# Optimization experiments

Measured on AMD Instinct MI355X. Metric: run time of the kernel, lower is better.

## Reference

```python
import jax, jax.numpy as jnp
import numpy as np
import math

B = 128      # bandwidth
BATCH = 2048 # flat batch (samples x channels)


def _dlt_weights(Bv):
    # Driscoll-Healy quadrature weights, length 2B
    k = np.arange(2 * Bv)
    p = np.arange(Bv)
    C = 2.0 / Bv * np.sin(np.pi * (2 * k + 1) / (4.0 * Bv))
    S = np.sin(np.outer(2 * k + 1, 2 * p + 1) * np.pi / (4.0 * Bv))  # [2B,B]
    return C * (S @ (1.0 / (2 * p + 1)))


def _idct_matrix(N):
    k = np.arange(N)[:, None]
    n = np.arange(N)[None, :]
    DI = np.cos(np.pi * n * (k + 0.5) / N)
    DI[:, 0] *= np.sqrt(1.0 / N)
    DI[:, 1:] *= np.sqrt(2.0 / N)
    return DI


def _idst_matrix(N):
    k = np.arange(N)[:, None]
    n = np.arange(N)[None, :]
    DI = np.sin(np.pi * (n + 1) * (k + 0.5) / N)
    DI[:, N - 1] = (-1.0) ** np.arange(N)
    DI[:, :N - 1] *= np.sqrt(2.0 / N)
    DI[:, N - 1] *= np.sqrt(1.0 / N)
    return DI


def _little_half(Bv):
    # Wigner little-d at beta=pi/2 via 3-term recurrence (vectorized over m,n)
    Bm1 = Bv - 1
    s2 = np.sqrt(2.0)
    d = np.zeros((Bv, 2 * Bv - 1, 2 * Bv - 1))
    d[0, Bm1, Bm1] = 1.0
    d[1, Bm1 - 1, Bm1 - 1] = 0.5
    d[1, Bm1 - 1, Bm1] = 1.0 / s2
    d[1, Bm1 - 1, Bm1 + 1] = 0.5
    d[1, Bm1, Bm1 - 1] = -1.0 / s2
    d[1, Bm1, Bm1 + 1] = 1.0 / s2
    d[1, Bm1 + 1, Bm1 - 1] = 0.5
    d[1, Bm1 + 1, Bm1] = -1.0 / s2
    d[1, Bm1 + 1, Bm1 + 1] = 0.5
    for l in range(2, Bv):
        m = np.arange(l).astype(np.float64)
        M, Nn = np.meshgrid(m, m, indexing='ij')
        denom = (l - 1.0) * np.sqrt((l - M) * (l + M) * (l - Nn) * (l + Nn))
        c1 = (1.0 - 2.0 * l) * M * Nn / denom
        c2 = -l * np.sqrt(((l - 1.0) ** 2 - M ** 2) * ((l - 1.0) ** 2 - Nn ** 2)) / denom
        d[l, Bm1:Bm1 + l, Bm1:Bm1 + l] = (c1 * d[l - 1, Bm1:Bm1 + l, Bm1:Bm1 + l]
                                          + c2 * d[l - 2, Bm1:Bm1 + l, Bm1:Bm1 + l])
        mm = np.arange(l + 1)
        lnV = np.array([0.5 * (math.lgamma(2 * l + 1) - math.lgamma(l + mi + 1)
                               - math.lgamma(l - mi + 1)) - l * math.log(2.0) for mi in mm])
        v = np.exp(lnV)
        d[l, Bm1 + mm, Bm1 + l] = v
        d[l, Bm1 + l, Bm1 + mm] = ((-1.0) ** (l - mm)) * v
        # symmetry fill (write order a1, a2, a3 reproduces torch loop semantics)
        sub = d[l, Bm1:Bm1 + l + 1, Bm1:Bm1 + l + 1].copy()
        M2, N2 = np.meshgrid(np.arange(l + 1), np.arange(l + 1), indexing='ij')
        a1 = ((-1.0) ** (M2 - N2)) * sub
        a2 = ((-1.0) ** (l - N2)) * sub
        a3 = ((-1.0) ** (l + M2)) * sub
        a1[0, 0] = sub[0, 0]
        a2[0, 0] = sub[0, 0]
        a3[0, 0] = sub[0, 0]
        d[l, Bm1 - l:Bm1 + 1, Bm1 - l:Bm1 + 1] = a1[::-1, ::-1]
        d[l, Bm1 - l:Bm1 + 1, Bm1:Bm1 + l + 1] = a2[::-1, :]
        d[l, Bm1:Bm1 + l + 1, Bm1 - l:Bm1 + 1] = a3[:, ::-1]
    return d


def _wigner_coeffs(Bv, d):
    Bm1 = Bv - 1
    N = 2 * Bv
    D = np.zeros((Bv, Bv, N))
    for m in range(Bv):
        for l in range(m, Bv):
            if m % 2 == 0:
                n = np.arange(l + 1)
                c = np.sqrt((2 * l + 1) / 2.0) * np.where(n == 0, np.sqrt(N), np.sqrt(2.0 * N))
                if m % 4 == 2:
                    c = -c
                coeff = c * d[l, n + Bm1, Bm1 - m] * d[l, n + Bm1, Bm1]
                coeff = np.where(np.abs(coeff) > 1e-15, coeff, 0.0)
                D[m, l, :l + 1] = coeff
            else:
                n = np.arange(l)  # n == l gives 0
                if l > 0:
                    c = np.sqrt((2 * l + 1) / 2.0) * np.sqrt(2.0 * N)
                    if m % 4 == 1:
                        c = -c
                    coeff = c * d[l, n + 1 + Bm1, Bm1 - m] * d[l, n + 1 + Bm1, Bm1]
                    coeff = np.where(np.abs(coeff) > 1e-15, coeff, 0.0)
                    D[m, l, :l] = coeff
    return D


def _buffers(Bv):
    N = 2 * Bv
    Wd = np.diag(_dlt_weights(Bv))
    XFc = Wd @ _idct_matrix(N)   # weighted DCT matrix (applied as x @ XFc)
    XFs = Wd @ _idst_matrix(N)   # weighted DST matrix
    D = _wigner_coeffs(Bv, _little_half(Bv))
    cm = ((-1.0) ** (Bv - 1)) * np.sqrt(1.0 / (2.0 * np.pi))  # Cm[B-1] scalar
    return XFc, XFs, D, cm


def setup_inputs() -> dict:
    key = jax.random.key(0)
    psiHat = jax.random.normal(key, (BATCH, B, 2 * B), dtype=jnp.float32)
    XFc, XFs, D, cm = _buffers(B)
    return {
        'psiHat': psiHat,
        'cm': jnp.float32(cm),
        'XFc': jnp.asarray(XFc, dtype=jnp.float32),
        'XFs': jnp.asarray(XFs, dtype=jnp.float32),
        'D': jnp.asarray(D, dtype=jnp.float32),
    }


def reference(psiHat, cm, XFc, XFs, D):
    # psiHat: [batch, B, 2B]; XFc/XFs: [2B, 2B]; D: [B, B, 2B]
    psi = psiHat * cm  # Cm[B-1:] broadcasts as a scalar
    # F.linear with weight = XF.T  ==  x @ XF on the last axis
    psi = psi.at[:, 0::2, :].set(jnp.einsum('bmi,ij->bmj', psi[:, 0::2, :], XFc))
    psi = psi.at[:, 1::2, :].set(jnp.einsum('bmi,ij->bmj', psi[:, 1::2, :], XFs))
    # per-order-m block matmul against Wigner coefficient blocks
    return jnp.einsum('bmi,moi->bmo', psi, D)
```

## Files before the change

### kernel.cpp

```cpp
#include <hip/hip_runtime.h>


typedef __attribute__((ext_vector_type(8))) short short8;
typedef __attribute__((ext_vector_type(4))) float f32x4;

#define NBATCH 2048
#define NM 128
#define NI 256
#define NO 128
#define BPACK_M 32768

__device__ __forceinline__ unsigned short f2bf(float f) {
  unsigned int u = __builtin_bit_cast(unsigned int, f);
  u += 0x7FFFu + ((u >> 16) & 1u);
  return (unsigned short)(u >> 16);
}

__device__ __forceinline__ short8 cvt8(float4 a, float4 b, float s) {
  short8 v;
  v[0] = (short)f2bf(s * a.x); v[1] = (short)f2bf(s * a.y);
  v[2] = (short)f2bf(s * a.z); v[3] = (short)f2bf(s * a.w);
  v[4] = (short)f2bf(s * b.x); v[5] = (short)f2bf(s * b.y);
  v[6] = (short)f2bf(s * b.z); v[7] = (short)f2bf(s * b.w);
  return v;
}

__global__ __launch_bounds__(256) void e_kernel(
    const float* __restrict__ XFc, const float* __restrict__ XFs,
    const float* __restrict__ D, const float* __restrict__ cmp,
    unsigned short* __restrict__ Bpack)
{
  const int m = blockIdx.x >> 1;
  const int ihalf = blockIdx.x & 1;
  const int tid = threadIdx.x;
  const int lane = tid & 63;
  const int w = tid >> 6;
  const int lr = lane & 15;
  const int lg = lane >> 4;
  const float cm = cmp[0];
  const float* __restrict__ Xp = (m & 1) ? XFs : XFc;
  const float* __restrict__ Dm = D + (size_t)m * (NO * NI);
  const int i0 = ihalf * 128 + w * 32;

  f32x4 acc[2][8];
#pragma unroll
  for (int a = 0; a < 2; a++)
#pragma unroll
    for (int b = 0; b < 8; b++) acc[a][b] = (f32x4)0.f;

  for (int kk = 0; kk < NI; kk += 32) {
    const int kb = kk + lg * 8;
    short8 af[2];
#pragma unroll
    for (int rf = 0; rf < 2; rf++) {
      const float* ap = Xp + (size_t)(i0 + rf * 16 + lr) * NI + kb;
      float4 x0 = *(const float4*)ap;
      float4 x1 = *(const float4*)(ap + 4);
      af[rf] = cvt8(x0, x1, cm);
    }
    short8 bf[8];
#pragma unroll
    for (int cf = 0; cf < 8; cf++) {
      const float* bp = Dm + (size_t)(cf * 16 + lr) * NI + kb;
      float4 x0 = *(const float4*)bp;
      float4 x1 = *(const float4*)(bp + 4);
      bf[cf] = cvt8(x0, x1, 1.0f);
    }
#pragma unroll
    for (int rf = 0; rf < 2; rf++)
#pragma unroll
      for (int cf = 0; cf < 8; cf++)
        acc[rf][cf] = __builtin_amdgcn_mfma_f32_16x16x32_bf16(
            af[rf], bf[cf], acc[rf][cf], 0, 0, 0);
  }

  unsigned short* Bm = Bpack + (size_t)m * BPACK_M;
#pragma unroll
  for (int rf = 0; rf < 2; rf++) {
    const int t = (i0 + rf * 16) >> 5;
    const int L = ((2 * rf + (lg >> 1)) & 3) * 16 + lr;
#pragma unroll
    for (int cf = 0; cf < 8; cf++) {
      ushort4 pk;
      pk.x = f2bf(acc[rf][cf][0]);
      pk.y = f2bf(acc[rf][cf][1]);
      pk.z = f2bf(acc[rf][cf][2]);
      pk.w = f2bf(acc[rf][cf][3]);
      *(ushort4*)(Bm + (size_t)(t * 8 + cf) * 512 + L * 8 + (lg & 1) * 4) = pk;
    }
  }
}

__global__ __launch_bounds__(256) void fdlt_main(
    const float* __restrict__ psiHat,
    const unsigned short* __restrict__ Bpack,
    float* __restrict__ out)
{
  const int m = blockIdx.x;
  const int tid = threadIdx.x;
  const int lane = tid & 63;
  const int w = tid >> 6;
  const int b0 = blockIdx.y * 128 + w * 32;
  const int lr = lane & 15;
  const int lg = lane >> 4;

  f32x4 acc[2][8];
#pragma unroll
  for (int a = 0; a < 2; a++)
#pragma unroll
    for (int b = 0; b < 8; b++) acc[a][b] = (f32x4)0.f;

  const unsigned short* __restrict__ Bm = Bpack + (size_t)m * BPACK_M;
  const float* arow0 = psiHat + ((size_t)(b0 + lr) * NM + m) * NI + lg * 8;
  const float* arow1 = psiHat + ((size_t)(b0 + 16 + lr) * NM + m) * NI + lg * 8;

#pragma unroll
  for (int half = 0; half < 2; half++) {
    float4 xa[16];
#pragma unroll
    for (int tt = 0; tt < 4; tt++) {
      const int kb = (half * 4 + tt) * 32;
      xa[tt * 2]         = *(const float4*)(arow0 + kb);
      xa[tt * 2 + 1]     = *(const float4*)(arow0 + kb + 4);
      xa[8 + tt * 2]     = *(const float4*)(arow1 + kb);
      xa[8 + tt * 2 + 1] = *(const float4*)(arow1 + kb + 4);
    }
    __builtin_amdgcn_sched_barrier(0);

    short8 af[2][4];
#pragma unroll
    for (int rf = 0; rf < 2; rf++)
#pragma unroll
      for (int tt = 0; tt < 4; tt++)
        af[rf][tt] = cvt8(xa[rf * 8 + tt * 2], xa[rf * 8 + tt * 2 + 1], 1.0f);

#pragma unroll
    for (int tt = 0; tt < 4; tt++) {
      const int t = half * 4 + tt;
      short8 bf[8];
#pragma unroll
      for (int cf = 0; cf < 8; cf++)
        bf[cf] = *(const short8*)(Bm + (size_t)(t * 8 + cf) * 512 + lane * 8);
#pragma unroll
      for (int rf = 0; rf < 2; rf++)
#pragma unroll
        for (int cf = 0; cf < 8; cf++)
          acc[rf][cf] = __builtin_amdgcn_mfma_f32_16x16x32_bf16(
              af[rf][tt], bf[cf], acc[rf][cf], 0, 0, 0);
    }
  }

#pragma unroll
  for (int rf = 0; rf < 2; rf++)
#pragma unroll
    for (int cf = 0; cf < 8; cf++) {
      const int o = cf * 16 + lr;
#pragma unroll
      for (int r = 0; r < 4; r++) {
        const int b = b0 + rf * 16 + lg * 4 + r;
        out[((size_t)b * NM + m) * NO + o] = acc[rf][cf][r];
      }
    }
}

extern "C" void kernel_launch(void* const* d_in, const int* in_sizes, int n_in,
                              void* d_out, int out_size, void* d_ws, size_t ws_size,
                              hipStream_t stream) {
  const float* psiHat = (const float*)d_in[0];
  const float* cm     = (const float*)d_in[1];
  const float* XFc    = (const float*)d_in[2];
  const float* XFs    = (const float*)d_in[3];
  const float* D      = (const float*)d_in[4];
  float* out = (float*)d_out;
  unsigned short* Bpack = (unsigned short*)d_ws;

  e_kernel<<<256, 256, 0, stream>>>(XFc, XFs, D, cm, Bpack);
  fdlt_main<<<dim3(NM, NBATCH / 128), 256, 0, stream>>>(psiHat, Bpack, out);
}
```

Before: 119.9 us.

## Software-pipeline psiHat and B-fragment loads against MFMA in main kernel

Restructures the main kernel's K loop into an explicit software pipeline. It prefetches the second half of the psiHat rows while the first half is converted, and double-buffers the packed B fragments so each tile's loads are issued before the previous tile's MFMAs. Scheduling barriers pin this order, and launch bounds now request 2 blocks per SM. Keeping more data live in flight raises register pressure, which may conflict with the occupancy hint or cause spills.

New measurement: 120.2 us. About the same (+0.2%).

```diff
diff --git a/kernel.cpp b/kernel.cpp
--- a/kernel.cpp
+++ b/kernel.cpp
@@ -91,7 +91,23 @@
   }
 }
 
-__global__ __launch_bounds__(256) void fdlt_main(
+#define LOADB(BUF, t)                                                   \
+  _Pragma("unroll")                                                     \
+  for (int cf = 0; cf < 8; cf++)                                        \
+    BUF[cf] = *(const short8*)(Bm + ((t) * 8 + cf) * 512 + lane * 8);
+
+#define SB __builtin_amdgcn_sched_barrier(0)
+
+#define MFMA8(A0, A1, BUF)                                              \
+  _Pragma("unroll")                                                     \
+  for (int cf = 0; cf < 8; cf++) {                                      \
+    acc[0][cf] = __builtin_amdgcn_mfma_f32_16x16x32_bf16(               \
+        A0, BUF[cf], acc[0][cf], 0, 0, 0);                              \
+    acc[1][cf] = __builtin_amdgcn_mfma_f32_16x16x32_bf16(               \
+        A1, BUF[cf], acc[1][cf], 0, 0, 0);                              \
+  }
+
+__global__ __launch_bounds__(256, 2) void fdlt_main(
     const float* __restrict__ psiHat,
     const unsigned short* __restrict__ Bpack,
     float* __restrict__ out)
@@ -112,43 +128,53 @@
 
   const unsigned short* __restrict__ Bm = Bpack + (size_t)m * BPACK_M;
   const float* arow0 = psiHat + ((size_t)(b0 + lr) * NM + m) * NI + lg * 8;
-  const float* arow1 = psiHat + ((size_t)(b0 + 16 + lr) * NM + m) * NI + lg * 8;
-
-#pragma unroll
-  for (int half = 0; half < 2; half++) {
-    float4 xa[16];
-#pragma unroll
-    for (int tt = 0; tt < 4; tt++) {
-      const int kb = (half * 4 + tt) * 32;
-      xa[tt * 2]         = *(const float4*)(arow0 + kb);
-      xa[tt * 2 + 1]     = *(const float4*)(arow0 + kb + 4);
-      xa[8 + tt * 2]     = *(const float4*)(arow1 + kb);
-      xa[8 + tt * 2 + 1] = *(const float4*)(arow1 + kb + 4);
-    }
-    __builtin_amdgcn_sched_barrier(0);
-
-    short8 af[2][4];
-#pragma unroll
-    for (int rf = 0; rf < 2; rf++)
-#pragma unroll
-      for (int tt = 0; tt < 4; tt++)
-        af[rf][tt] = cvt8(xa[rf * 8 + tt * 2], xa[rf * 8 + tt * 2 + 1], 1.0f);
-
-#pragma unroll
-    for (int tt = 0; tt < 4; tt++) {
-      const int t = half * 4 + tt;
-      short8 bf[8];
-#pragma unroll
-      for (int cf = 0; cf < 8; cf++)
-        bf[cf] = *(const short8*)(Bm + (size_t)(t * 8 + cf) * 512 + lane * 8);
-#pragma unroll
-      for (int rf = 0; rf < 2; rf++)
-#pragma unroll
-        for (int cf = 0; cf < 8; cf++)
-          acc[rf][cf] = __builtin_amdgcn_mfma_f32_16x16x32_bf16(
-              af[rf][tt], bf[cf], acc[rf][cf], 0, 0, 0);
-    }
-  }
+  const float* arow1 = arow0 + (size_t)16 * NM * NI;
+
+  float4 xa0[16];
+#pragma unroll
+  for (int tt = 0; tt < 4; tt++) {
+    xa0[tt * 2]         = *(const float4*)(arow0 + tt * 32);
+    xa0[tt * 2 + 1]     = *(const float4*)(arow0 + tt * 32 + 4);
+    xa0[8 + tt * 2]     = *(const float4*)(arow1 + tt * 32);
+    xa0[8 + tt * 2 + 1] = *(const float4*)(arow1 + tt * 32 + 4);
+  }
+  SB;
+
+  short8 af0[2][4];
+#pragma unroll
+  for (int tt = 0; tt < 4; tt++) {
+    af0[0][tt] = cvt8(xa0[tt * 2], xa0[tt * 2 + 1], 1.0f);
+    af0[1][tt] = cvt8(xa0[8 + tt * 2], xa0[8 + tt * 2 + 1], 1.0f);
+  }
+
+  short8 bf0[8], bf1[8];
+  LOADB(bf0, 0);
+  float4 xa1[16];
+#pragma unroll
+  for (int tt = 0; tt < 4; tt++) {
+    xa1[tt * 2]         = *(const float4*)(arow0 + (4 + tt) * 32);
+    xa1[tt * 2 + 1]     = *(const float4*)(arow0 + (4 + tt) * 32 + 4);
+    xa1[8 + tt * 2]     = *(const float4*)(arow1 + (4 + tt) * 32);
+    xa1[8 + tt * 2 + 1] = *(const float4*)(arow1 + (4 + tt) * 32 + 4);
+  }
+  SB;
+
+  LOADB(bf1, 1); SB; MFMA8(af0[0][0], af0[1][0], bf0);
+  LOADB(bf0, 2); SB; MFMA8(af0[0][1], af0[1][1], bf1);
+  LOADB(bf1, 3); SB; MFMA8(af0[0][2], af0[1][2], bf0);
+  LOADB(bf0, 4); SB; MFMA8(af0[0][3], af0[1][3], bf1);
+
+  short8 af1[2][4];
+#pragma unroll
+  for (int tt = 0; tt < 4; tt++) {
+    af1[0][tt] = cvt8(xa1[tt * 2], xa1[tt * 2 + 1], 1.0f);
+    af1[1][tt] = cvt8(xa1[8 + tt * 2], xa1[8 + tt * 2 + 1], 1.0f);
+  }
+
+  LOADB(bf1, 5); SB; MFMA8(af1[0][0], af1[1][0], bf0);
+  LOADB(bf0, 6); SB; MFMA8(af1[0][1], af1[1][1], bf1);
+  LOADB(bf1, 7); SB; MFMA8(af1[0][2], af1[1][2], bf0);
+                 SB; MFMA8(af1[0][3], af1[1][3], bf1);
 
 #pragma unroll
   for (int rf = 0; rf < 2; rf++)
```

## Stage psiHat rows into swizzled LDS via direct global-to-LDS loads

Applied to the files above, without the earlier changes.

The main kernel now copies each block's 64 batch rows of psiHat into shared memory with global_load_lds DMA, using an XOR swizzle to avoid bank conflicts. Each wave handles 16 rows instead of 32, so the grid doubles and occupancy is raised via launch bounds. B fragments are double-buffered across k-steps. The aim is to hide global load latency for the strided psiHat reads and expose more parallelism. In exchange it uses 64KB of LDS per block and reloads each B fragment once per 16 rows instead of once per 32.

After: 117.4 us. -2.1%, faster.

```diff
diff --git a/kernel.cpp b/kernel.cpp
--- a/kernel.cpp
+++ b/kernel.cpp
@@ -9,6 +9,9 @@
 #define NI 256
 #define NO 128
 #define BPACK_M 32768
+
+#define GLB(p) ((const __attribute__((address_space(1))) void*)(p))
+#define LDS(p) ((__attribute__((address_space(3))) void*)(p))
 
 __device__ __forceinline__ unsigned short f2bf(float f) {
   unsigned int u = __builtin_bit_cast(unsigned int, f);
@@ -91,76 +94,75 @@
   }
 }
 
-__global__ __launch_bounds__(256) void fdlt_main(
+#define LOADB(BUF, t)                                                   \
+  _Pragma("unroll")                                                     \
+  for (int cf = 0; cf < 8; cf++)                                        \
+    BUF[cf] = *(const short8*)(Bm + ((t) * 8 + cf) * 512 + lane * 8);
+
+#define SB __builtin_amdgcn_sched_barrier(0)
+
+__global__ __launch_bounds__(256, 2) void fdlt_main(
     const float* __restrict__ psiHat,
     const unsigned short* __restrict__ Bpack,
     float* __restrict__ out)
 {
+  __shared__ float As_f[64 * 256];
   const int m = blockIdx.x;
   const int tid = threadIdx.x;
   const int lane = tid & 63;
   const int w = tid >> 6;
-  const int b0 = blockIdx.y * 128 + w * 32;
+  const int b0 = blockIdx.y * 64;
   const int lr = lane & 15;
   const int lg = lane >> 4;
+  char* As = (char*)As_f;
 
-  f32x4 acc[2][8];
 #pragma unroll
-  for (int a = 0; a < 2; a++)
+  for (int s = 0; s < 16; s++) {
+    const int r = s * 4 + w;
+    const int fofs = ((((lane >> 1) ^ (r & 7)) << 3) + ((lane & 1) << 2));
+    const float* src = psiHat + ((size_t)(b0 + r) * NM + m) * NI + fofs;
+    __builtin_amdgcn_global_load_lds(GLB(src), LDS(As + r * 1024), 16, 0, 0);
+  }
+
+  f32x4 acc[8];
 #pragma unroll
-    for (int b = 0; b < 8; b++) acc[a][b] = (f32x4)0.f;
+  for (int b = 0; b < 8; b++) acc[b] = (f32x4)0.f;
 
   const unsigned short* __restrict__ Bm = Bpack + (size_t)m * BPACK_M;
-  const float* arow0 = psiHat + ((size_t)(b0 + lr) * NM + m) * NI + lg * 8;
-  const float* arow1 = psiHat + ((size_t)(b0 + 16 + lr) * NM + m) * NI + lg * 8;
+
+  short8 bf0[8], bf1[8];
+  LOADB(bf0, 0);
+  SB;
+
+  __syncthreads();
+
+  const int arow = w * 16 + lr;
+  const char* Arow = As + arow * 1024;
+  const int rsw = lr & 7;
 
 #pragma unroll
-  for (int half = 0; half < 2; half++) {
-    float4 xa[16];
+  for (int t = 0; t < 8; t++) {
+    if (t < 7) { LOADB(((t & 1) ? bf0 : bf1), t + 1); SB; }
+    const int p = ((t * 4 + lg) ^ rsw) << 5;
+    float4 x0 = *(const float4*)(Arow + p);
+    float4 x1 = *(const float4*)(Arow + p + 16);
+    short8 af = cvt8(x0, x1, 1.0f);
+    const short8* bf = (t & 1) ? bf1 : bf0;
 #pragma unroll
-    for (int tt = 0; tt < 4; tt++) {
-      const int kb = (half * 4 + tt) * 32;
-      xa[tt * 2]         = *(const float4*)(arow0 + kb);
-      xa[tt * 2 + 1]     = *(const float4*)(arow0 + kb + 4);
-      xa[8 + tt * 2]     = *(const float4*)(arow1 + kb);
-      xa[8 + tt * 2 + 1] = *(const float4*)(arow1 + kb + 4);
-    }
-    __builtin_amdgcn_sched_barrier(0);
-
-    short8 af[2][4];
-#pragma unroll
-    for (int rf = 0; rf < 2; rf++)
-#pragma unroll
-      for (int tt = 0; tt < 4; tt++)
-        af[rf][tt] = cvt8(xa[rf * 8 + tt * 2], xa[rf * 8 + tt * 2 + 1], 1.0f);
-
-#pragma unroll
-    for (int tt = 0; tt < 4; tt++) {
-      const int t = half * 4 + tt;
-      short8 bf[8];
-#pragma unroll
-      for (int cf = 0; cf < 8; cf++)
-        bf[cf] = *(const short8*)(Bm + (size_t)(t * 8 + cf) * 512 + lane * 8);
-#pragma unroll
-      for (int rf = 0; rf < 2; rf++)
-#pragma unroll
-        for (int cf = 0; cf < 8; cf++)
-          acc[rf][cf] = __builtin_amdgcn_mfma_f32_16x16x32_bf16(
-              af[rf][tt], bf[cf], acc[rf][cf], 0, 0, 0);
-    }
+    for (int cf = 0; cf < 8; cf++)
+      acc[cf] = __builtin_amdgcn_mfma_f32_16x16x32_bf16(
+          af, bf[cf], acc[cf], 0, 0, 0);
   }
 
 #pragma unroll
-  for (int rf = 0; rf < 2; rf++)
+  for (int cf = 0; cf < 8; cf++) {
+    const int o = cf * 16 + lr;
 #pragma unroll
-    for (int cf = 0; cf < 8; cf++) {
-      const int o = cf * 16 + lr;
-#pragma unroll
-      for (int r = 0; r < 4; r++) {
-        const int b = b0 + rf * 16 + lg * 4 + r;
-        out[((size_t)b * NM + m) * NO + o] = acc[rf][cf][r];
-      }
+    for (int r = 0; r < 4; r++) {
+      const int b = b0 + w * 16 + lg * 4 + r;
+      out[((size_t)b * NM + m) * NO + o] = acc[cf][r];
     }
+  }
 }
 
 extern "C" void kernel_launch(void* const* d_in, const int* in_sizes, int n_in,
@@ -175,5 +177,5 @@
   unsigned short* Bpack = (unsigned short*)d_ws;
 
   e_kernel<<<256, 256, 0, stream>>>(XFc, XFs, D, cm, Bpack);
-  fdlt_main<<<dim3(NM, NBATCH / 128), 256, 0, stream>>>(psiHat, Bpack, out);
+  fdlt_main<<<dim3(NM, NBATCH / 64), 256, 0, stream>>>(psiHat, Bpack, out);
 }
```
